# Kernel optimization log

Measured on AMD Instinct MI355X. Metric: run time of the kernel, lower is better.

## Reference

```python
import jax, jax.numpy as jnp
import numpy as np

B, S, D = 2, 2048, 1024
H = 16
HD = D // H

def setup_inputs() -> dict:
    key = jax.random.key(0)
    ks = jax.random.split(key, 6)
    sc = 0.02
    return {
        'x': jax.random.normal(ks[0], (B, S, D), jnp.float32),
        'Wq': jax.random.normal(ks[1], (D, D), jnp.float32) * sc,
        'Wk': jax.random.normal(ks[2], (D, D), jnp.float32) * sc,
        'Wv': jax.random.normal(ks[3], (D, D), jnp.float32) * sc,
        'Wo': jax.random.normal(ks[4], (D, D), jnp.float32) * sc,
        'bo': jnp.zeros((D,), jnp.float32),
    }

def reference(x, Wq, Wk, Wv, Wo, bo):
    b, s, d_in = x.shape
    # torch Linear: y = x @ W.T
    q = jnp.einsum('bsd,ed->bse', x, Wq)
    k = jnp.einsum('bsd,ed->bse', x, Wk)
    v = jnp.einsum('bsd,ed->bse', x, Wv)
    # [b, h, s, hd]
    q = q.reshape(b, s, H, HD).transpose(0, 2, 1, 3)
    k = k.reshape(b, s, H, HD).transpose(0, 2, 1, 3)
    v = v.reshape(b, s, H, HD).transpose(0, 2, 1, 3)
    # NOTE: original divides by sqrt(d_out), not sqrt(head_dim)
    scores = jnp.einsum('bhqd,bhkd->bhqk', q, k) / jnp.sqrt(jnp.float32(D))
    causal = jnp.tril(jnp.ones((s, s), dtype=bool))  # True = keep
    scores = jnp.where(causal[None, None], scores, -jnp.inf)
    attn = jax.nn.softmax(scores, axis=-1)
    ctx = jnp.einsum('bhqk,bhkd->bhqd', attn, v)
    ctx = ctx.transpose(0, 2, 1, 3).reshape(b, s, D)
    return jnp.einsum('bsd,ed->bse', ctx, Wo) + bo
```

## Files before the change

kernel.cpp:

```cpp
#include <hip/hip_runtime.h>
#include <hip/hip_bf16.h>
#include <stdint.h>

typedef unsigned short u16;
typedef __attribute__((ext_vector_type(8))) short short8;
typedef __attribute__((ext_vector_type(4))) float f32x4;
typedef __attribute__((ext_vector_type(16))) float f32x16;
typedef __attribute__((ext_vector_type(4))) u16 u16x4;

#define NB 2
#define NS 2048
#define ND 1024
#define NH 16
#define NM 4096

#define QSCALE 0.045084220f
#define SM_SHIFT 8.0f

#if __has_builtin(__builtin_amdgcn_exp2f)
#define EXP2(x) __builtin_amdgcn_exp2f(x)
#else
__device__ __forceinline__ float __exp2_asm(float x){
  float r;
  asm("v_exp_f32 %0, %1" : "=v"(r) : "v"(x));
  return r;
}
#define EXP2(x) __exp2_asm(x)
#endif
#if __has_builtin(__builtin_amdgcn_rcpf)
#define RCP(x) __builtin_amdgcn_rcpf(x)
#else
#define RCP(x) (1.0f / (x))
#endif

__device__ __forceinline__ u16 f2bf(float f){
  union { float f; unsigned u; } v; v.f = f;
  unsigned r = v.u + 0x7fff + ((v.u >> 16) & 1);
  return (u16)(r >> 16);
}

__device__ __forceinline__ unsigned cvtpk(float lo, float hi){
  unsigned r;
  asm("v_cvt_pk_bf16_f32 %0, %1, %2" : "=v"(r) : "v"(lo), "v"(hi));
  return r;
}

__device__ __forceinline__ void pl32swap(unsigned &e, unsigned &o){
  asm("v_permlane32_swap_b32 %0, %1" : "+v"(e), "+v"(o));
}

__device__ __forceinline__ void gload_lds16(const u16* g, u16* l){
  __builtin_amdgcn_global_load_lds(
      (const __attribute__((address_space(1))) unsigned int*)g,
      (__attribute__((address_space(3))) unsigned int*)l, 16, 0, 0);
}

__device__ __forceinline__ f32x16 mfma32(short8 a, short8 b, f32x16 c){
  return __builtin_amdgcn_mfma_f32_32x32x16_bf16(a, b, c, 0, 0, 0);
}

__global__ void cvt_all(const float* __restrict__ x,
                        const float* __restrict__ wq, const float* __restrict__ wk,
                        const float* __restrict__ wv, const float* __restrict__ wo,
                        u16* __restrict__ xb, u16* __restrict__ wqb, u16* __restrict__ wkb,
                        u16* __restrict__ wvb, u16* __restrict__ wob){
  int ib = blockIdx.x;
  const float* s; u16* d; int off;
  if (ib < 4096){ s = x; d = xb; off = ib; }
  else {
    int t = ib - 4096, sel = t >> 10;
    off = t & 1023;
    s = (sel == 0) ? wq : (sel == 1) ? wk : (sel == 2) ? wv : wo;
    d = (sel == 0) ? wqb : (sel == 1) ? wkb : (sel == 2) ? wvb : wob;
  }
  int i = (off * 256 + threadIdx.x) * 4;
  float4 v = *(const float4*)(s + i);
  u16x4 pk = { f2bf(v.x), f2bf(v.y), f2bf(v.z), f2bf(v.w) };
  *(u16x4*)(d + i) = pk;
}

__device__ __forceinline__ void gemm_core(
    const u16* __restrict__ A, const u16* __restrict__ W,
    int m0, int n0, u16* lsA, u16* lsB, f32x4 acc[4][4])
{
  const int tid = threadIdx.x;
  const int l   = tid & 63;
  const int wr  = (tid >> 7) & 1;
  const int wc  = (tid >> 6) & 1;
  const int lr  = l & 15;
  const int lkb = (l >> 4) << 4;
  const int sr  = tid >> 3;
  const int scb = (tid & 7) << 4;

  for (int kt = 0; kt < 16; ++kt){
    const int k0 = kt << 6;
    #pragma unroll
    for (int i = 0; i < 4; ++i){
      int r   = (i << 5) + sr;
      int cbs = scb ^ ((r & 7) << 4);
      gload_lds16(&A[(size_t)(m0 + r) * ND + k0 + (cbs >> 1)], &lsA[r * 64 + (scb >> 1)]);
      gload_lds16(&W[(size_t)(n0 + r) * ND + k0 + (cbs >> 1)], &lsB[r * 64 + (scb >> 1)]);
    }
    __syncthreads();

    short8 af[4][2], bf[4][2];
    #pragma unroll
    for (int m16 = 0; m16 < 4; ++m16){
      int r  = (wr << 6) + (m16 << 4) + lr;
      int rx = (r & 7) << 4;
      #pragma unroll
      for (int ks = 0; ks < 2; ++ks){
        int off = r * 128 + (((ks << 6) + lkb) ^ rx);
        af[m16][ks] = *(const short8*)((const char*)lsA + off);
      }
    }
    #pragma unroll
    for (int n16 = 0; n16 < 4; ++n16){
      int r  = (wc << 6) + (n16 << 4) + lr;
      int rx = (r & 7) << 4;
      #pragma unroll
      for (int ks = 0; ks < 2; ++ks){
        int off = r * 128 + (((ks << 6) + lkb) ^ rx);
        bf[n16][ks] = *(const short8*)((const char*)lsB + off);
      }
    }
    #pragma unroll
    for (int m16 = 0; m16 < 4; ++m16)
      #pragma unroll
      for (int n16 = 0; n16 < 4; ++n16){
        acc[m16][n16] = __builtin_amdgcn_mfma_f32_16x16x32_bf16(af[m16][0], bf[n16][0], acc[m16][n16], 0, 0, 0);
        acc[m16][n16] = __builtin_amdgcn_mfma_f32_16x16x32_bf16(af[m16][1], bf[n16][1], acc[m16][n16], 0, 0, 0);
      }
    __syncthreads();
  }
}

__global__ __launch_bounds__(256) void gemm_qkv(
    const u16* __restrict__ xb,
    const u16* __restrict__ Wqb, const u16* __restrict__ Wkb, const u16* __restrict__ Wvb,
    u16* __restrict__ Qo, u16* __restrict__ Ko, u16* __restrict__ Vt)
{
  __shared__ u16 lsA[128*64];
  __shared__ u16 lsB[128*64];
  const int z = blockIdx.z;
  const u16* W = (z == 0) ? Wqb : (z == 1) ? Wkb : Wvb;
  const int m0 = blockIdx.x << 7, n0 = blockIdx.y << 7;
  f32x4 acc[4][4] = {};
  gemm_core(xb, W, m0, n0, lsA, lsB, acc);

  const int l  = threadIdx.x & 63;
  const int wr = (threadIdx.x >> 7) & 1, wc = (threadIdx.x >> 6) & 1;
  const int rb = m0 + (wr << 6) + ((l >> 4) << 2);
  const int cb = n0 + (wc << 6) + (l & 15);

  if (z < 2){
    const float sc = (z == 0) ? QSCALE : 1.0f;
    u16* C = (z == 0) ? Qo : Ko;
    #pragma unroll
    for (int m16 = 0; m16 < 4; ++m16)
      #pragma unroll
      for (int n16 = 0; n16 < 4; ++n16)
        #pragma unroll
        for (int r = 0; r < 4; ++r)
          C[(size_t)(rb + (m16 << 4) + r) * ND + cb + (n16 << 4)] = f2bf(acc[m16][n16][r] * sc);
  } else {
    #pragma unroll
    for (int m16 = 0; m16 < 4; ++m16){
      int srow = rb + (m16 << 4);
      int bi = srow >> 11, s = srow & 2047;
      #pragma unroll
      for (int n16 = 0; n16 < 4; ++n16){
        int col = cb + (n16 << 4);
        u16x4 pk = { f2bf(acc[m16][n16][0]), f2bf(acc[m16][n16][1]),
                     f2bf(acc[m16][n16][2]), f2bf(acc[m16][n16][3]) };
        *(u16x4*)&Vt[((size_t)(bi * 16 + (col >> 6)) * 64 + (col & 63)) * 2048 + s] = pk;
      }
    }
  }
}

__global__ __launch_bounds__(256) void gemm_out(
    const u16* __restrict__ ctxb, const u16* __restrict__ Wob,
    const float* __restrict__ bo, float* __restrict__ out)
{
  __shared__ u16 lsA[64*64];
  __shared__ u16 lsB[128*64];
  const int m0 = blockIdx.x << 6, n0 = blockIdx.y << 7;
  const int tid = threadIdx.x;
  const int l = tid & 63;
  const int w = tid >> 6;
  const int lr = l & 15;
  const int lkb = (l >> 4) << 4;
  const int rl = tid >> 3, ch = tid & 7;

  f32x4 acc[4][2] = {};

  for (int kt = 0; kt < 16; ++kt){
    const int k0 = kt << 6;
    #pragma unroll
    for (int k = 0; k < 2; ++k){
      int rr = rl + (k << 5);
      int cs = ch ^ (rr & 7);
      gload_lds16(&ctxb[(size_t)(m0 + rr) * ND + k0 + cs * 8], &lsA[rr * 64 + ch * 8]);
    }
    #pragma unroll
    for (int k = 0; k < 4; ++k){
      int rr = rl + (k << 5);
      int cs = ch ^ (rr & 7);
      gload_lds16(&Wob[(size_t)(n0 + rr) * ND + k0 + cs * 8], &lsB[rr * 64 + ch * 8]);
    }
    __syncthreads();

    short8 af[4][2], bf[2][2];
    #pragma unroll
    for (int m16 = 0; m16 < 4; ++m16){
      int r  = (m16 << 4) + lr;
      int rx = (r & 7) << 4;
      #pragma unroll
      for (int ks = 0; ks < 2; ++ks)
        af[m16][ks] = *(const short8*)((const char*)lsA + r * 128 + (((ks << 6) + lkb) ^ rx));
    }
    #pragma unroll
    for (int n16 = 0; n16 < 2; ++n16){
      int r  = (w << 5) + (n16 << 4) + lr;
      int rx = (r & 7) << 4;
      #pragma unroll
      for (int ks = 0; ks < 2; ++ks)
        bf[n16][ks] = *(const short8*)((const char*)lsB + r * 128 + (((ks << 6) + lkb) ^ rx));
    }
    #pragma unroll
    for (int m16 = 0; m16 < 4; ++m16)
      #pragma unroll
      for (int n16 = 0; n16 < 2; ++n16){
        acc[m16][n16] = __builtin_amdgcn_mfma_f32_16x16x32_bf16(af[m16][0], bf[n16][0], acc[m16][n16], 0, 0, 0);
        acc[m16][n16] = __builtin_amdgcn_mfma_f32_16x16x32_bf16(af[m16][1], bf[n16][1], acc[m16][n16], 0, 0, 0);
      }
    __syncthreads();
  }

  const int rb = m0 + ((l >> 4) << 2);
  const int cb = n0 + (w << 5) + lr;
  #pragma unroll
  for (int m16 = 0; m16 < 4; ++m16)
    #pragma unroll
    for (int n16 = 0; n16 < 2; ++n16)
      #pragma unroll
      for (int r = 0; r < 4; ++r){
        int col = cb + (n16 << 4);
        out[(size_t)(rb + (m16 << 4) + r) * ND + col] = acc[m16][n16][r] + bo[col];
      }
}

__device__ __forceinline__ void stage_tile(const u16* src, int srcStride, u16* lds, int tid){
  const int rl = tid >> 3;
  const int ch = tid & 7;
  const int cs = ch ^ (rl & 7);
  gload_lds16(&src[(size_t)rl * srcStride + cs * 8],        &lds[rl * 64 + ch * 8]);
  gload_lds16(&src[(size_t)(rl + 32) * srcStride + cs * 8], &lds[(rl + 32) * 64 + ch * 8]);
}

__device__ __forceinline__ void qk_tile(const u16* lsKt, const short8 qf[4],
                                        int q5, int hi, f32x16 &s0, f32x16 &s1){
  const char* Kc = (const char*)lsKt;
  const int swz = q5 & 7;
  f32x16 a = {}, b = {};
  __builtin_amdgcn_s_setprio(1);
  #pragma unroll
  for (int ks = 0; ks < 4; ++ks){
    int c0 = ((2 * ks + hi) ^ swz) << 4;
    short8 k0 = *(const short8*)(Kc + q5 * 128 + c0);
    short8 k1 = *(const short8*)(Kc + (q5 + 32) * 128 + c0);
    a = mfma32(k0, qf[ks], a);
    b = mfma32(k1, qf[ks], b);
  }
  __builtin_amdgcn_s_setprio(0);
  s0 = a; s1 = b;
}

__device__ __forceinline__ void sm_pv(f32x16 s0, f32x16 s1, const u16* lsVt,
                                      int t, int qb, int qgl, int q5, int hi,
                                      float &l_r, f32x16 &accA, f32x16 &accB){
  if (t * 64 + 63 > qb){
    #pragma unroll
    for (int r = 0; r < 16; ++r){
      int kl = t * 64 + (r & 3) + 8 * (r >> 2) + 4 * hi;
      if (kl > qgl)      s0[r] = -3e38f;
      if (kl + 32 > qgl) s1[r] = -3e38f;
    }
  }

  #pragma unroll
  for (int r = 0; r < 16; ++r){
    s0[r] = EXP2(s0[r] - SM_SHIFT);
    s1[r] = EXP2(s1[r] - SM_SHIFT);
  }
  float sm[16];
  #pragma unroll
  for (int r = 0; r < 16; ++r) sm[r] = s0[r] + s1[r];
  #pragma unroll
  for (int stp = 8; stp > 0; stp >>= 1)
    #pragma unroll
    for (int r = 0; r < stp; ++r) sm[r] += sm[r + stp];
  l_r += sm[0];

  unsigned pw[2][4][2];
  #pragma unroll
  for (int g = 0; g < 4; ++g){
    pw[0][g][0] = cvtpk(s0[4*g],     s0[4*g + 1]);
    pw[0][g][1] = cvtpk(s0[4*g + 2], s0[4*g + 3]);
    pw[1][g][0] = cvtpk(s1[4*g],     s1[4*g + 1]);
    pw[1][g][1] = cvtpk(s1[4*g + 2], s1[4*g + 3]);
  }
  #pragma unroll
  for (int m = 0; m < 2; ++m)
    #pragma unroll
    for (int kp = 0; kp < 2; ++kp)
      #pragma unroll
      for (int i = 0; i < 2; ++i)
        pl32swap(pw[m][2*kp][i], pw[m][2*kp + 1][i]);

  const char* Vc = (const char*)lsVt;
  const int swz = q5 & 7;
  __builtin_amdgcn_s_setprio(1);
  #pragma unroll
  for (int ks = 0; ks < 4; ++ks){
    const int m = ks >> 1, kp = ks & 1;
    union { unsigned u[4]; short8 s8; } pa;
    pa.u[0] = pw[m][2*kp][0];
    pa.u[1] = pw[m][2*kp][1];
    pa.u[2] = pw[m][2*kp + 1][0];
    pa.u[3] = pw[m][2*kp + 1][1];
    int c0 = ((2 * ks + hi) ^ swz) << 4;
    short8 v0 = *(const short8*)(Vc + q5 * 128 + c0);
    short8 v1 = *(const short8*)(Vc + (q5 + 32) * 128 + c0);
    accA = mfma32(pa.s8, v0, accA);
    accB = mfma32(pa.s8, v1, accB);
  }
  __builtin_amdgcn_s_setprio(0);
}

#define SUBITER(T, SC0, SC1, SN0, SN1)                                            \
  {                                                                               \
    const int t_ = (T);                                                           \
    if (t_ + 3 <= tb){                                                            \
      stage_tile(&Kb0[(size_t)(t_ + 3) * 64 * ND], ND, lsK[(t_ + 3) & 3], tid);   \
      stage_tile(&Vb0[(t_ + 3) * 64],              NS, lsV[(t_ + 3) & 3], tid);   \
    }                                                                             \
    if (t_ + 1 <= nc) qk_tile(lsK[(t_ + 1) & 3], qf, q5, hi, SN0, SN1);           \
    if (t_ <= nc)     sm_pv(SC0, SC1, lsV[t_ & 3], t_, qb, qgl, q5, hi,           \
                            l_r, accA, accB);                                     \
    if (t_ + 3 <= tb) asm volatile("s_waitcnt vmcnt(4)" ::: "memory");            \
    else              asm volatile("s_waitcnt vmcnt(0)" ::: "memory");            \
    __builtin_amdgcn_sched_barrier(0);                                            \
    __builtin_amdgcn_s_barrier();                                                 \
    __builtin_amdgcn_sched_barrier(0);                                            \
  }

__global__ __launch_bounds__(256, 2) void attn_kernel(
    const u16* __restrict__ Q, const u16* __restrict__ K,
    const u16* __restrict__ Vt, u16* __restrict__ ctx)
{
  __shared__ __align__(16) u16 lsK[4][64*64];
  __shared__ __align__(16) u16 lsV[4][64*64];

  const int bid = blockIdx.x;
  const int xcd = bid & 7;
  const int j   = bid >> 3;
  const int strm = (j & 31) >> 3;
  const int idx  = j & 7;
  const int st   = (j < 32) ? (15 - idx) : idx;
  const int bh   = xcd + 8 * strm;
  const int b = bh >> 4, h = bh & 15;
  const int tid = threadIdx.x;
  const int l = tid & 63, w = tid >> 6;
  const int q5 = l & 31, hi = l >> 5;
  const int qb   = st * 128 + w * 32;
  const int qgl  = qb + q5;
  const int nc   = (qb + 31) >> 6;
  const int tb   = 2 * st + 1;

  const u16* Kb0 = &K[(size_t)(b * NS) * ND + h * 64];
  const u16* Vb0 = &Vt[(size_t)bh * 64 * NS];

  short8 qf[4];
  {
    const u16* Qrow = &Q[(size_t)(b * NS + qgl) * ND + h * 64 + hi * 8];
    #pragma unroll
    for (int ks = 0; ks < 4; ++ks)
      qf[ks] = *(const short8*)&Qrow[ks * 16];
  }

  float l_r = 0.f;
  f32x16 accA = {}, accB = {};
  f32x16 sA0, sA1, sB0, sB1;

  stage_tile(Kb0, ND, lsK[0], tid);
  stage_tile(Vb0, NS, lsV[0], tid);
  stage_tile(&Kb0[(size_t)64 * ND], ND, lsK[1], tid);
  stage_tile(&Vb0[64],              NS, lsV[1], tid);
  if (2 <= tb){
    stage_tile(&Kb0[(size_t)128 * ND], ND, lsK[2], tid);
    stage_tile(&Vb0[128],              NS, lsV[2], tid);
    asm volatile("s_waitcnt vmcnt(4)" ::: "memory");
  } else {
    asm volatile("s_waitcnt vmcnt(0)" ::: "memory");
  }
  __builtin_amdgcn_sched_barrier(0);
  __builtin_amdgcn_s_barrier();
  __builtin_amdgcn_sched_barrier(0);
  qk_tile(lsK[0], qf, q5, hi, sA0, sA1);

  #pragma unroll 1
  for (int t = 0; t <= tb; t += 2){
    SUBITER(t,     sA0, sA1, sB0, sB1);
    SUBITER(t + 1, sB0, sB1, sA0, sA1);
  }

  float l_full = l_r + __shfl_xor(l_r, 32);
  float inv = RCP(l_full);
  #pragma unroll
  for (int r = 0; r < 16; ++r){
    int qrow = (r & 3) + 8 * (r >> 2) + 4 * hi;
    float iv = __shfl(inv, (l & 32) | qrow, 64);
    u16* crow = &ctx[(size_t)(b * NS + qb + qrow) * ND + h * 64 + q5];
    crow[0]  = f2bf(accA[r] * iv);
    crow[32] = f2bf(accB[r] * iv);
  }
}

extern "C" void kernel_launch(void* const* d_in, const int* in_sizes, int n_in,
                              void* d_out, int out_size, void* d_ws, size_t ws_size,
                              hipStream_t stream)
{
  const float* x  = (const float*)d_in[0];
  const float* Wq = (const float*)d_in[1];
  const float* Wk = (const float*)d_in[2];
  const float* Wv = (const float*)d_in[3];
  const float* Wo = (const float*)d_in[4];
  const float* bo = (const float*)d_in[5];
  float* out = (float*)d_out;
  char* ws = (char*)d_ws;

  u16* xb  = (u16*)(ws);
  u16* Wqb = (u16*)(ws + (8u  << 20));
  u16* Wkb = (u16*)(ws + (10u << 20));
  u16* Wvb = (u16*)(ws + (12u << 20));
  u16* Wob = (u16*)(ws + (14u << 20));
  u16* Qb  = (u16*)(ws + (16u << 20));
  u16* Kb  = (u16*)(ws + (24u << 20));
  u16* Vtb = (u16*)(ws + (32u << 20));
  u16* Cb  = (u16*)(ws + (40u << 20));

  cvt_all<<<8192, 256, 0, stream>>>(x, Wq, Wk, Wv, Wo, xb, Wqb, Wkb, Wvb, Wob);

  gemm_qkv<<<dim3(32, 8, 3), 256, 0, stream>>>(xb, Wqb, Wkb, Wvb, Qb, Kb, Vtb);
  attn_kernel<<<512, 256, 0, stream>>>(Qb, Kb, Vtb, Cb);
  gemm_out<<<dim3(64, 8), 256, 0, stream>>>(Cb, Wob, bo, out);
}
```

Before: 113.2 us.

## Double-buffer LDS tiles in QKV projection GEMM to overlap loads with MFMA

Replaces the shared gemm_core call in the QKV projection kernel with an inlined loop that keeps two LDS buffers. The next K-tile is loaded straight from global memory into LDS while MFMAs run on the current tile. Wave priority is raised around the MFMA block, and a single barrier per iteration replaces the two-sync pattern. This doubles LDS use to 64KB per block, which may lower occupancy, in exchange for hiding global load latency.

```diff
diff --git a/kernel.cpp b/kernel.cpp
--- a/kernel.cpp
+++ b/kernel.cpp
@@ -140,16 +140,82 @@
     const u16* __restrict__ Wqb, const u16* __restrict__ Wkb, const u16* __restrict__ Wvb,
     u16* __restrict__ Qo, u16* __restrict__ Ko, u16* __restrict__ Vt)
 {
-  __shared__ u16 lsA[128*64];
-  __shared__ u16 lsB[128*64];
+  __shared__ u16 lsA[2][128*64];
+  __shared__ u16 lsB[2][128*64];
   const int z = blockIdx.z;
   const u16* W = (z == 0) ? Wqb : (z == 1) ? Wkb : Wvb;
   const int m0 = blockIdx.x << 7, n0 = blockIdx.y << 7;
+
+  const int tid = threadIdx.x;
+  const int l   = tid & 63;
+  const int wr  = (tid >> 7) & 1;
+  const int wc  = (tid >> 6) & 1;
+  const int lr  = l & 15;
+  const int lkb = (l >> 4) << 4;
+  const int sr  = tid >> 3;
+  const int scb = (tid & 7) << 4;
+
   f32x4 acc[4][4] = {};
-  gemm_core(xb, W, m0, n0, lsA, lsB, acc);
-
-  const int l  = threadIdx.x & 63;
-  const int wr = (threadIdx.x >> 7) & 1, wc = (threadIdx.x >> 6) & 1;
+
+  auto stage = [&](int kt, int bufi){
+    const int k0 = kt << 6;
+    #pragma unroll
+    for (int i = 0; i < 4; ++i){
+      int r   = (i << 5) + sr;
+      int cbs = scb ^ ((r & 7) << 4);
+      gload_lds16(&xb[(size_t)(m0 + r) * ND + k0 + (cbs >> 1)], &lsA[bufi][r * 64 + (scb >> 1)]);
+      gload_lds16(&W[(size_t)(n0 + r) * ND + k0 + (cbs >> 1)],  &lsB[bufi][r * 64 + (scb >> 1)]);
+    }
+  };
+
+  stage(0, 0);
+  asm volatile("s_waitcnt vmcnt(0)" ::: "memory");
+  __builtin_amdgcn_sched_barrier(0);
+  __builtin_amdgcn_s_barrier();
+  __builtin_amdgcn_sched_barrier(0);
+
+  #pragma unroll 1
+  for (int kt = 0; kt < 16; ++kt){
+    const int cur = kt & 1;
+    if (kt < 15) stage(kt + 1, cur ^ 1);
+
+    short8 af[4][2], bf[4][2];
+    #pragma unroll
+    for (int m16 = 0; m16 < 4; ++m16){
+      int r  = (wr << 6) + (m16 << 4) + lr;
+      int rx = (r & 7) << 4;
+      #pragma unroll
+      for (int ks = 0; ks < 2; ++ks){
+        int off = r * 128 + (((ks << 6) + lkb) ^ rx);
+        af[m16][ks] = *(const short8*)((const char*)&lsA[cur][0] + off);
+      }
+    }
+    #pragma unroll
+    for (int n16 = 0; n16 < 4; ++n16){
+      int r  = (wc << 6) + (n16 << 4) + lr;
+      int rx = (r & 7) << 4;
+      #pragma unroll
+      for (int ks = 0; ks < 2; ++ks){
+        int off = r * 128 + (((ks << 6) + lkb) ^ rx);
+        bf[n16][ks] = *(const short8*)((const char*)&lsB[cur][0] + off);
+      }
+    }
+    __builtin_amdgcn_s_setprio(1);
+    #pragma unroll
+    for (int m16 = 0; m16 < 4; ++m16)
+      #pragma unroll
+      for (int n16 = 0; n16 < 4; ++n16){
+        acc[m16][n16] = __builtin_amdgcn_mfma_f32_16x16x32_bf16(af[m16][0], bf[n16][0], acc[m16][n16], 0, 0, 0);
+        acc[m16][n16] = __builtin_amdgcn_mfma_f32_16x16x32_bf16(af[m16][1], bf[n16][1], acc[m16][n16], 0, 0, 0);
+      }
+    __builtin_amdgcn_s_setprio(0);
+
+    asm volatile("s_waitcnt vmcnt(0)" ::: "memory");
+    __builtin_amdgcn_sched_barrier(0);
+    __builtin_amdgcn_s_barrier();
+    __builtin_amdgcn_sched_barrier(0);
+  }
+
   const int rb = m0 + (wr << 6) + ((l >> 4) << 2);
   const int cb = n0 + (wc << 6) + (l & 15);
 
```

New measurement: 110.1 us. -2.7%, faster.

## Double-buffer LDS tiles in QKV and output GEMMs to overlap loads with MFMA

Applied to the files above, without the earlier changes.

Both projection GEMMs now keep two LDS buffers and issue the global-to-LDS loads for the next K tile before computing on the current one, with one barrier per iteration instead of two. The MFMA block is wrapped in s_setprio to favour math waves. This aims to hide global load latency behind matrix work, at the cost of doubled LDS use (64KB for the QKV kernel), which may lower occupancy.

```diff
diff --git a/kernel.cpp b/kernel.cpp
--- a/kernel.cpp
+++ b/kernel.cpp
@@ -79,10 +79,17 @@
   *(u16x4*)(d + i) = pk;
 }
 
-__device__ __forceinline__ void gemm_core(
-    const u16* __restrict__ A, const u16* __restrict__ W,
-    int m0, int n0, u16* lsA, u16* lsB, f32x4 acc[4][4])
+__global__ __launch_bounds__(256) void gemm_qkv(
+    const u16* __restrict__ xb,
+    const u16* __restrict__ Wqb, const u16* __restrict__ Wkb, const u16* __restrict__ Wvb,
+    u16* __restrict__ Qo, u16* __restrict__ Ko, u16* __restrict__ Vt)
 {
+  __shared__ u16 lsA[2][128*64];
+  __shared__ u16 lsB[2][128*64];
+  const int z = blockIdx.z;
+  const u16* W = (z == 0) ? Wqb : (z == 1) ? Wkb : Wvb;
+  const int m0 = blockIdx.x << 7, n0 = blockIdx.y << 7;
+
   const int tid = threadIdx.x;
   const int l   = tid & 63;
   const int wr  = (tid >> 7) & 1;
@@ -92,16 +99,29 @@
   const int sr  = tid >> 3;
   const int scb = (tid & 7) << 4;
 
-  for (int kt = 0; kt < 16; ++kt){
+  f32x4 acc[4][4] = {};
+
+  auto stage = [&](int kt, int bufi){
     const int k0 = kt << 6;
     #pragma unroll
     for (int i = 0; i < 4; ++i){
       int r   = (i << 5) + sr;
       int cbs = scb ^ ((r & 7) << 4);
-      gload_lds16(&A[(size_t)(m0 + r) * ND + k0 + (cbs >> 1)], &lsA[r * 64 + (scb >> 1)]);
-      gload_lds16(&W[(size_t)(n0 + r) * ND + k0 + (cbs >> 1)], &lsB[r * 64 + (scb >> 1)]);
-    }
-    __syncthreads();
+      gload_lds16(&xb[(size_t)(m0 + r) * ND + k0 + (cbs >> 1)], &lsA[bufi][r * 64 + (scb >> 1)]);
+      gload_lds16(&W[(size_t)(n0 + r) * ND + k0 + (cbs >> 1)],  &lsB[bufi][r * 64 + (scb >> 1)]);
+    }
+  };
+
+  stage(0, 0);
+  asm volatile("s_waitcnt vmcnt(0)" ::: "memory");
+  __builtin_amdgcn_sched_barrier(0);
+  __builtin_amdgcn_s_barrier();
+  __builtin_amdgcn_sched_barrier(0);
+
+  #pragma unroll 1
+  for (int kt = 0; kt < 16; ++kt){
+    const int cur = kt & 1;
+    if (kt < 15) stage(kt + 1, cur ^ 1);
 
     short8 af[4][2], bf[4][2];
     #pragma unroll
@@ -111,7 +131,7 @@
       #pragma unroll
       for (int ks = 0; ks < 2; ++ks){
         int off = r * 128 + (((ks << 6) + lkb) ^ rx);
-        af[m16][ks] = *(const short8*)((const char*)lsA + off);
+        af[m16][ks] = *(const short8*)((const char*)&lsA[cur][0] + off);
       }
     }
     #pragma unroll
@@ -121,9 +141,10 @@
       #pragma unroll
       for (int ks = 0; ks < 2; ++ks){
         int off = r * 128 + (((ks << 6) + lkb) ^ rx);
-        bf[n16][ks] = *(const short8*)((const char*)lsB + off);
-      }
-    }
+        bf[n16][ks] = *(const short8*)((const char*)&lsB[cur][0] + off);
+      }
+    }
+    __builtin_amdgcn_s_setprio(1);
     #pragma unroll
     for (int m16 = 0; m16 < 4; ++m16)
       #pragma unroll
@@ -131,25 +152,14 @@
         acc[m16][n16] = __builtin_amdgcn_mfma_f32_16x16x32_bf16(af[m16][0], bf[n16][0], acc[m16][n16], 0, 0, 0);
         acc[m16][n16] = __builtin_amdgcn_mfma_f32_16x16x32_bf16(af[m16][1], bf[n16][1], acc[m16][n16], 0, 0, 0);
       }
-    __syncthreads();
-  }
-}
-
-__global__ __launch_bounds__(256) void gemm_qkv(
-    const u16* __restrict__ xb,
-    const u16* __restrict__ Wqb, const u16* __restrict__ Wkb, const u16* __restrict__ Wvb,
-    u16* __restrict__ Qo, u16* __restrict__ Ko, u16* __restrict__ Vt)
-{
-  __shared__ u16 lsA[128*64];
-  __shared__ u16 lsB[128*64];
-  const int z = blockIdx.z;
-  const u16* W = (z == 0) ? Wqb : (z == 1) ? Wkb : Wvb;
-  const int m0 = blockIdx.x << 7, n0 = blockIdx.y << 7;
-  f32x4 acc[4][4] = {};
-  gemm_core(xb, W, m0, n0, lsA, lsB, acc);
-
-  const int l  = threadIdx.x & 63;
-  const int wr = (threadIdx.x >> 7) & 1, wc = (threadIdx.x >> 6) & 1;
+    __builtin_amdgcn_s_setprio(0);
+
+    asm volatile("s_waitcnt vmcnt(0)" ::: "memory");
+    __builtin_amdgcn_sched_barrier(0);
+    __builtin_amdgcn_s_barrier();
+    __builtin_amdgcn_sched_barrier(0);
+  }
+
   const int rb = m0 + (wr << 6) + ((l >> 4) << 2);
   const int cb = n0 + (wc << 6) + (l & 15);
 
@@ -183,8 +193,8 @@
     const u16* __restrict__ ctxb, const u16* __restrict__ Wob,
     const float* __restrict__ bo, float* __restrict__ out)
 {
-  __shared__ u16 lsA[64*64];
-  __shared__ u16 lsB[128*64];
+  __shared__ u16 lsA[2][64*64];
+  __shared__ u16 lsB[2][128*64];
   const int m0 = blockIdx.x << 6, n0 = blockIdx.y << 7;
   const int tid = threadIdx.x;
   const int l = tid & 63;
@@ -195,21 +205,32 @@
 
   f32x4 acc[4][2] = {};
 
-  for (int kt = 0; kt < 16; ++kt){
+  auto stage = [&](int kt, int bufi){
     const int k0 = kt << 6;
     #pragma unroll
     for (int k = 0; k < 2; ++k){
       int rr = rl + (k << 5);
       int cs = ch ^ (rr & 7);
-      gload_lds16(&ctxb[(size_t)(m0 + rr) * ND + k0 + cs * 8], &lsA[rr * 64 + ch * 8]);
+      gload_lds16(&ctxb[(size_t)(m0 + rr) * ND + k0 + cs * 8], &lsA[bufi][rr * 64 + ch * 8]);
     }
     #pragma unroll
     for (int k = 0; k < 4; ++k){
       int rr = rl + (k << 5);
       int cs = ch ^ (rr & 7);
-      gload_lds16(&Wob[(size_t)(n0 + rr) * ND + k0 + cs * 8], &lsB[rr * 64 + ch * 8]);
-    }
-    __syncthreads();
+      gload_lds16(&Wob[(size_t)(n0 + rr) * ND + k0 + cs * 8], &lsB[bufi][rr * 64 + ch * 8]);
+    }
+  };
+
+  stage(0, 0);
+  asm volatile("s_waitcnt vmcnt(0)" ::: "memory");
+  __builtin_amdgcn_sched_barrier(0);
+  __builtin_amdgcn_s_barrier();
+  __builtin_amdgcn_sched_barrier(0);
+
+  #pragma unroll 1
+  for (int kt = 0; kt < 16; ++kt){
+    const int cur = kt & 1;
+    if (kt < 15) stage(kt + 1, cur ^ 1);
 
     short8 af[4][2], bf[2][2];
     #pragma unroll
@@ -218,7 +239,7 @@
       int rx = (r & 7) << 4;
       #pragma unroll
       for (int ks = 0; ks < 2; ++ks)
-        af[m16][ks] = *(const short8*)((const char*)lsA + r * 128 + (((ks << 6) + lkb) ^ rx));
+        af[m16][ks] = *(const short8*)((const char*)&lsA[cur][0] + r * 128 + (((ks << 6) + lkb) ^ rx));
     }
     #pragma unroll
     for (int n16 = 0; n16 < 2; ++n16){
@@ -226,8 +247,9 @@
       int rx = (r & 7) << 4;
       #pragma unroll
       for (int ks = 0; ks < 2; ++ks)
-        bf[n16][ks] = *(const short8*)((const char*)lsB + r * 128 + (((ks << 6) + lkb) ^ rx));
-    }
+        bf[n16][ks] = *(const short8*)((const char*)&lsB[cur][0] + r * 128 + (((ks << 6) + lkb) ^ rx));
+    }
+    __builtin_amdgcn_s_setprio(1);
     #pragma unroll
     for (int m16 = 0; m16 < 4; ++m16)
       #pragma unroll
@@ -235,7 +257,12 @@
         acc[m16][n16] = __builtin_amdgcn_mfma_f32_16x16x32_bf16(af[m16][0], bf[n16][0], acc[m16][n16], 0, 0, 0);
         acc[m16][n16] = __builtin_amdgcn_mfma_f32_16x16x32_bf16(af[m16][1], bf[n16][1], acc[m16][n16], 0, 0, 0);
       }
-    __syncthreads();
+    __builtin_amdgcn_s_setprio(0);
+
+    asm volatile("s_waitcnt vmcnt(0)" ::: "memory");
+    __builtin_amdgcn_sched_barrier(0);
+    __builtin_amdgcn_s_barrier();
+    __builtin_amdgcn_sched_barrier(0);
   }
 
   const int rb = m0 + ((l >> 4) << 2);
```

Measured after the change: 113.1 us. About the same (-0.0%).
